# Kernel optimization log

Hardware: AMD Instinct MI355X
Metric: run time of the kernel (lower is better)

Reference implementation:

```python
import jax, jax.numpy as jnp
import numpy as np

B, S, A = 65536, 376, 17
H1, H2, K = 400, 300, 15
MAX_ACTION = 1.0


def setup_inputs() -> dict:
    key = jax.random.key(0)
    ks = jax.random.split(key, 16)

    def lin(kw, fan_in, fan_out):
        lim = 1.0 / np.sqrt(fan_in)
        k1, k2 = jax.random.split(kw)
        W = jax.random.uniform(k1, (fan_in, fan_out), jnp.float32, -lim, lim)
        b = jax.random.uniform(k2, (fan_out,), jnp.float32, -lim, lim)
        return W, b

    W1, b1 = lin(ks[0], S, H1)
    W2, b2 = lin(ks[1], H1, H2)
    Wmu, bmu = lin(ks[2], H2, A)
    Wlv, blv = lin(ks[3], H2, A)
    Wu, bu = lin(ks[4], H2, K * A)
    Ww, bw = lin(ks[5], H2, K * A)
    Wb, bb = lin(ks[6], H2, K)
    x = jax.random.normal(ks[7], (B, S), jnp.float32)
    eps = jax.random.normal(ks[8], (B, A), jnp.float32)
    return dict(x=x, eps=eps, W1=W1, b1=b1, W2=W2, b2=b2, Wmu=Wmu, bmu=bmu,
                Wlv=Wlv, blv=blv, Wu=Wu, bu=bu, Ww=Ww, bw=bw, Wb=Wb, bb=bb)


def _flow_chain(action, u, w, b):
    # u, w: (K, B, A); b: (K, B). Sequential planar flow -> lax.scan over K.
    def step(carry, uwb):
        z, ldj = carry
        u_k, w_k, b_k = uwb
        uw = jnp.sum(w_k * u_k, -1)                       # (B,)
        m_uw = -1.0 + jax.nn.softplus(uw)
        w_norm_sq = jnp.sum(w_k * w_k, -1)
        u_hat = u_k + ((m_uw - uw) / w_norm_sq)[:, None] * w_k  # invertibility reparam
        wzb = jnp.sum(w_k * z, -1) + b_k                  # (B,)
        t = jnp.tanh(wzb)
        z_new = z + u_hat * t[:, None]
        psi_u = jnp.sum(w_k * u_hat, -1) * (1.0 - t * t)  # psi^T u_hat
        ldj_new = ldj + jnp.log(jnp.abs(1.0 + psi_u))
        return (z_new, ldj_new), None

    init = (action, jnp.zeros(action.shape[0], action.dtype))
    (z_fin, ldj), _ = jax.lax.scan(step, init, (u, w, b))
    return z_fin, ldj


def reference(x, eps, W1, b1, W2, b2, Wmu, bmu, Wlv, blv, Wu, bu, Ww, bw, Wb, bb):
    h = jax.nn.relu(x @ W1 + b1)
    h = jax.nn.relu(h @ W2 + b2)
    mu = MAX_ACTION * jnp.tanh(h @ Wmu + bmu)
    log_var = MAX_ACTION * jnp.tanh(h @ Wlv + blv)
    std = jnp.exp(log_var)                 # torch code uses log_var.exp() as the scale
    action = mu + std * eps                # rsample

    u = (h @ Wu + bu).reshape(B, K, A).transpose(1, 0, 2)   # (K, B, A)
    w = (h @ Ww + bw).reshape(B, K, A).transpose(1, 0, 2)   # (K, B, A)
    b = (h @ Wb + bb).T                                      # (K, B)

    final_action, log_det_j = _flow_chain(action, u, w, b)

    # Normal(mu, std).log_prob(action) summed over action dim; (action-mu)/std == eps
    log_2pi = jnp.float32(np.log(2.0 * np.pi))
    log_prob = jnp.sum(-0.5 * eps * eps - log_var - 0.5 * log_2pi, axis=-1)
    log_prob_final = log_prob - log_det_j
    prob_final = jnp.exp(log_prob_final)
    return final_action, prob_final, log_prob_final
```

## Files before the change

kernel.cpp:

```cpp
#include <hip/hip_runtime.h>

typedef unsigned short ushort_t;
typedef unsigned int uint_t;
typedef __bf16 bf16x8 __attribute__((ext_vector_type(8)));
typedef float f32x4 __attribute__((ext_vector_type(4)));

#define B_ROWS 65536

#define KT1 12
#define NT1 30
#define KTC1 15
#define KI2 13
#define NT2 20
#define KTC2 10
#define KI3 10
#define NT3 40
#define LDC3 640

#define SZ1 (NT1 * KT1 * 512)
#define SZ2 (NT2 * KI2 * 512)
#define SZ3 (NT3 * KI3 * 512)

__device__ inline float bf2f(ushort_t u) {
    union { uint_t i; float f; } x; x.i = ((uint_t)u) << 16; return x.f;
}
__device__ inline ushort_t f2bf(float f) {
    uint_t u = __float_as_uint(f);
    return (ushort_t)((u + 0x7FFFu + ((u >> 16) & 1u)) >> 16);
}
__device__ inline uint_t pack2(float a, float b) {
    return (uint_t)f2bf(a) | ((uint_t)f2bf(b) << 16);
}
__device__ inline float fast_tanh(float x) {
    float e = __expf(2.f * x);
    return 1.f - 2.f / (e + 1.f);
}
__device__ inline void gl2lds16(const ushort_t* g, ushort_t* l) {
    __builtin_amdgcn_global_load_lds(
        (const __attribute__((address_space(1))) uint_t*)g,
        (__attribute__((address_space(3))) uint_t*)l, 16, 0, 0);
}

__global__ void pack_kernel(const float* __restrict__ W1, const float* __restrict__ W2,
                            const float* __restrict__ Wmu, const float* __restrict__ Wlv,
                            const float* __restrict__ Wu, const float* __restrict__ Ww,
                            const float* __restrict__ Wb,
                            const float* __restrict__ b1, const float* __restrict__ b2,
                            const float* __restrict__ bmu, const float* __restrict__ blv,
                            const float* __restrict__ bu, const float* __restrict__ bw,
                            const float* __restrict__ bb,
                            ushort_t* __restrict__ W1t, ushort_t* __restrict__ W2t,
                            ushort_t* __restrict__ Wht,
                            float* __restrict__ b1p, float* __restrict__ b2p,
                            float* __restrict__ bHp)
{
    int i = blockIdx.x * 256 + threadIdx.x;
    if (i < SZ1) {
        int t = i >> 9, pos = i & 511;
        int l = pos >> 3, j = pos & 7;
        int n = (t / KT1) * 16 + (l & 15);
        int k = (t % KT1) * 32 + (l >> 4) * 8 + j;
        W1t[i] = (n < 400 && k < 376) ? f2bf(W1[k * 400 + n]) : (ushort_t)0;
    } else if (i < SZ1 + SZ2) {
        int i2 = i - SZ1;
        int t = i2 >> 9, pos = i2 & 511;
        int l = pos >> 3, j = pos & 7;
        int n = (t / KI2) * 16 + (l & 15);
        int k = (t % KI2) * 32 + (l >> 4) * 8 + j;
        W2t[i2] = (n < 300 && k < 400) ? f2bf(W2[k * 300 + n]) : (ushort_t)0;
    } else if (i < SZ1 + SZ2 + SZ3) {
        int i3 = i - SZ1 - SZ2;
        int t = i3 >> 9, pos = i3 & 511;
        int l = pos >> 3, j = pos & 7;
        int n = (t / KI3) * 16 + (l & 15);
        int k = (t % KI3) * 32 + (l >> 4) * 8 + j;
        float v = 0.f;
        if (k < 300) {
            if      (n < 17)  v = Wmu[k * 17 + n];
            else if (n < 34)  v = Wlv[k * 17 + (n - 17)];
            else if (n < 289) v = Wu[k * 255 + (n - 34)];
            else if (n < 544) v = Ww[k * 255 + (n - 289)];
            else if (n < 559) v = Wb[k * 15 + (n - 544)];
        }
        Wht[i3] = f2bf(v);
    } else {
        int j = i - SZ1 - SZ2 - SZ3;
        if (j < 480) {
            b1p[j] = (j < 400) ? b1[j] : 0.f;
        } else if (j < 800) {
            int n = j - 480;
            b2p[n] = (n < 300) ? b2[n] : 0.f;
        } else if (j < 1440) {
            int n = j - 800;
            float v = 0.f;
            if      (n < 17)  v = bmu[n];
            else if (n < 34)  v = blv[n - 17];
            else if (n < 289) v = bu[n - 34];
            else if (n < 544) v = bw[n - 289];
            else if (n < 559) v = bb[n - 544];
            bHp[n] = v;
        }
    }
}

__global__ __launch_bounds__(256)
void cvt_kernel(const float* __restrict__ x, ushort_t* __restrict__ xt, int nUnits)
{
    int U = blockIdx.x * 256 + threadIdx.x;
    if (U >= nUnits) return;
    int t = U >> 6, l = U & 63;
    int rowblk = t / KT1, kblk = t - rowblk * KT1;
    long row = (long)rowblk * 16 + (l & 15);
    int k0 = kblk * 32 + (l >> 4) * 8;
    uint4 o = {0u, 0u, 0u, 0u};
    if (k0 + 8 <= 376) {
        const float4* p = reinterpret_cast<const float4*>(x + row * 376 + k0);
        float4 v0 = p[0], v1 = p[1];
        o.x = pack2(v0.x, v0.y); o.y = pack2(v0.z, v0.w);
        o.z = pack2(v1.x, v1.y); o.w = pack2(v1.z, v1.w);
    }
    reinterpret_cast<uint4*>(xt)[U] = o;
}

template<bool RELU, bool OUT_TILED>
__global__ __launch_bounds__(256)
void gemm_tile(const ushort_t* __restrict__ A, const ushort_t* __restrict__ Bt,
               const float* __restrict__ bias, ushort_t* __restrict__ C,
               int kTA, int kIters, int kTC)
{
    __shared__ ushort_t As[8 * 512];
    __shared__ ushort_t Bs[10 * 512];
    const int tid = threadIdx.x;
    const int lane = tid & 63, wv = tid >> 6;
    const int q = lane >> 4, l16 = lane & 15;
    const int nb0 = blockIdx.x * 10;
    const int rowblk0 = blockIdx.y * 8;

    f32x4 acc[2][10];
    #pragma unroll
    for (int r = 0; r < 2; ++r)
        #pragma unroll
        for (int c = 0; c < 10; ++c)
            acc[r][c] = (f32x4){0.f, 0.f, 0.f, 0.f};

    for (int kt = 0; kt < kIters; ++kt) {
        #pragma unroll
        for (int i = 0; i < 2; ++i) {
            int t = wv * 2 + i;
            gl2lds16(A + (((size_t)(rowblk0 + t) * kTA + kt) << 9) + lane * 8,
                     &As[t << 9]);
        }
        #pragma unroll
        for (int t2 = 0; t2 < 3; ++t2) {
            int t = wv + t2 * 4;
            if (t < 10)
                gl2lds16(Bt + (((size_t)(nb0 + t) * kIters + kt) << 9) + lane * 8,
                         &Bs[t << 9]);
        }
        __syncthreads();

        bf16x8 a0 = __builtin_bit_cast(bf16x8,
            *reinterpret_cast<const uint4*>(&As[((wv * 2 + 0) << 9) + lane * 8]));
        bf16x8 a1 = __builtin_bit_cast(bf16x8,
            *reinterpret_cast<const uint4*>(&As[((wv * 2 + 1) << 9) + lane * 8]));
        #pragma unroll
        for (int c = 0; c < 10; ++c) {
            bf16x8 b = __builtin_bit_cast(bf16x8,
                *reinterpret_cast<const uint4*>(&Bs[(c << 9) + lane * 8]));
            acc[0][c] = __builtin_amdgcn_mfma_f32_16x16x32_bf16(a0, b, acc[0][c], 0, 0, 0);
            acc[1][c] = __builtin_amdgcn_mfma_f32_16x16x32_bf16(a1, b, acc[1][c], 0, 0, 0);
        }
        __syncthreads();
    }

    #pragma unroll
    for (int r = 0; r < 2; ++r) {
        int rowblk = rowblk0 + wv * 2 + r;
        #pragma unroll
        for (int c = 0; c < 10; ++c) {
            int n = (nb0 + c) * 16 + l16;
            float bv = bias[n];
            #pragma unroll
            for (int reg = 0; reg < 4; ++reg) {
                float v = acc[r][c][reg] + bv;
                if (RELU) v = fmaxf(v, 0.f);
                int mrow = q * 4 + reg;
                if (OUT_TILED) {
                    size_t off = (((size_t)rowblk * kTC + (n >> 5)) << 9)
                               + (size_t)(((n >> 3) & 3) * 16 + mrow) * 8 + (n & 7);
                    C[off] = f2bf(v);
                } else {
                    long m = (long)rowblk * 16 + mrow;
                    C[m * (long)kTC + n] = f2bf(v);
                }
            }
        }
    }
}

#define FR 128

__global__ __launch_bounds__(FR)
void flow_kernel(const ushort_t* __restrict__ heads, const float* __restrict__ eps,
                 float* __restrict__ out, int rowBase, int B)
{
    __shared__ float lu[17 * (FR + 1)];
    __shared__ float lw[17 * (FR + 1)];
    __shared__ float le[17 * (FR + 1)];
    __shared__ float lb[FR];
    const int tid = threadIdx.x;
    const long row0 = (long)blockIdx.x * FR;
    const ushort_t* hbase = heads + row0 * LDC3;

    for (int idx = tid; idx < FR * 17; idx += FR) {
        int r = idx / 17, i = idx - r * 17;
        lu[i * (FR + 1) + r] = bf2f(hbase[(long)r * LDC3 + i]);
        lw[i * (FR + 1) + r] = bf2f(hbase[(long)r * LDC3 + 17 + i]);
        le[i * (FR + 1) + r] = eps[row0 * 17 + idx];
    }
    __syncthreads();

    float z[17];
    float lp = 0.f;
    #pragma unroll
    for (int i = 0; i < 17; ++i) {
        float mu = fast_tanh(lu[i * (FR + 1) + tid]);
        float lv = fast_tanh(lw[i * (FR + 1) + tid]);
        float ep = le[i * (FR + 1) + tid];
        z[i] = mu + __expf(lv) * ep;
        lp += -0.5f * ep * ep - lv - 0.918938533f;
    }

    float ldj = 0.f;
    for (int k = 0; k < 15; ++k) {
        __syncthreads();
        for (int idx = tid; idx < FR * 17; idx += FR) {
            int r = idx / 17, i = idx - r * 17;
            long rb = (long)r * LDC3;
            lu[i * (FR + 1) + r] = bf2f(hbase[rb + 34 + k * 17 + i]);
            lw[i * (FR + 1) + r] = bf2f(hbase[rb + 289 + k * 17 + i]);
        }
        lb[tid] = bf2f(hbase[(long)tid * LDC3 + 544 + k]);
        __syncthreads();

        float u[17], w[17];
        float uw = 0.f, w2 = 0.f, wz = 0.f;
        #pragma unroll
        for (int i = 0; i < 17; ++i) {
            u[i] = lu[i * (FR + 1) + tid];
            w[i] = lw[i * (FR + 1) + tid];
            uw += w[i] * u[i];
            w2 += w[i] * w[i];
            wz += w[i] * z[i];
        }
        float sp = (uw > 15.f) ? uw : __logf(1.f + __expf(uw));
        float m = sp - 1.f;
        float coef = (m - uw) / fmaxf(w2, 1e-20f);
        float t = fast_tanh(wz + lb[tid]);
        #pragma unroll
        for (int i = 0; i < 17; ++i)
            z[i] += (u[i] + coef * w[i]) * t;
        float psi = m * (1.f - t * t);
        ldj += __logf(fmaxf(fabsf(1.f + psi), 1e-30f));
    }

    const long g = rowBase + row0 + tid;
    #pragma unroll
    for (int i = 0; i < 17; ++i) out[g * 17 + i] = z[i];
    float lpf = lp - ldj;
    out[(long)B * 17 + g] = __expf(lpf);
    out[(long)B * 18 + g] = lpf;
}

extern "C" void kernel_launch(void* const* d_in, const int* in_sizes, int n_in,
                              void* d_out, int out_size, void* d_ws, size_t ws_size,
                              hipStream_t stream)
{
    const float* x   = (const float*)d_in[0];
    const float* eps = (const float*)d_in[1];
    float* out = (float*)d_out;

    const size_t wUS = (size_t)SZ1 + SZ2 + SZ3;
    const size_t fixedBytes = wUS * 2 + (480 + 320 + 640) * 4;
    int Mc = 2048;
    {
        const int cand[6] = {65536, 32768, 16384, 8192, 4096, 2048};
        for (int i = 0; i < 6; ++i) {
            size_t req = (size_t)cand[i] * 2048 + fixedBytes;
            if (req <= ws_size) { Mc = cand[i]; break; }
        }
    }

    ushort_t* region1 = (ushort_t*)d_ws;
    ushort_t* region2 = region1 + (size_t)Mc * 640;
    ushort_t* W1t = region2 + (size_t)Mc * 384;
    ushort_t* W2t = W1t + SZ1;
    ushort_t* Wht = W2t + SZ2;
    float* b1p = (float*)(Wht + SZ3);
    float* b2p = b1p + 480;
    float* bHp = b2p + 320;

    const int packN = SZ1 + SZ2 + SZ3 + 1440;
    pack_kernel<<<(packN + 255) / 256, 256, 0, stream>>>(
        (const float*)d_in[2],  (const float*)d_in[4],
        (const float*)d_in[6],  (const float*)d_in[8],
        (const float*)d_in[10], (const float*)d_in[12], (const float*)d_in[14],
        (const float*)d_in[3],  (const float*)d_in[5],
        (const float*)d_in[7],  (const float*)d_in[9],
        (const float*)d_in[11], (const float*)d_in[13], (const float*)d_in[15],
        W1t, W2t, Wht, b1p, b2p, bHp);

    const int nChunks = B_ROWS / Mc;
    const int nUnits = Mc * 48;
    for (int c = 0; c < nChunks; ++c) {
        const float* xc = x + (size_t)c * Mc * 376;
        cvt_kernel<<<(nUnits + 255) / 256, 256, 0, stream>>>(xc, region2, nUnits);
        gemm_tile<true, true><<<dim3(3, Mc / 128), 256, 0, stream>>>(
            region2, W1t, b1p, region1, KT1, KT1, KTC1);
        gemm_tile<true, true><<<dim3(2, Mc / 128), 256, 0, stream>>>(
            region1, W2t, b2p, region2, KTC1, KI2, KTC2);
        gemm_tile<false, false><<<dim3(4, Mc / 128), 256, 0, stream>>>(
            region2, Wht, bHp, region1, KTC2, KI3, LDC3);
        flow_kernel<<<Mc / FR, FR, 0, stream>>>(region1, eps + (size_t)c * Mc * 17,
                                                out, c * Mc, B_ROWS);
    }
}
```

Before: 375.8 us.

## Write head GEMM output in tiled layout and read it per-thread in flow kernel

The head GEMM now stores its output in the same tiled bf16 layout used by the earlier layers instead of a row-major 640-wide matrix. The flow kernel reads that layout directly: each thread loads 16-byte groups of 8 bf16 values for its own row. This replaces the shared-memory staging and the per-step __syncthreads. Each thread loads slightly more data than it needs (three groups per 17-element slice), and the fully unrolled K loop with 24-float buffers raises register pressure.

```diff
diff --git a/kernel.cpp b/kernel.cpp
--- a/kernel.cpp
+++ b/kernel.cpp
@@ -15,7 +15,7 @@
 #define KTC2 10
 #define KI3 10
 #define NT3 40
-#define LDC3 640
+#define LDH3 20
 
 #define SZ1 (NT1 * KT1 * 512)
 #define SZ2 (NT2 * KI2 * 512)
@@ -198,78 +198,85 @@
     }
 }
 
-#define FR 128
-
-__global__ __launch_bounds__(FR)
+__device__ inline void ld_group8(const ushort_t* hb, int g, float* dst) {
+    uint4 v = *reinterpret_cast<const uint4*>(hb + ((g >> 2) << 9) + ((g & 3) << 7));
+    uint_t q[4] = {v.x, v.y, v.z, v.w};
+    #pragma unroll
+    for (int m = 0; m < 4; ++m) {
+        dst[2 * m]     = __uint_as_float(q[m] << 16);
+        dst[2 * m + 1] = __uint_as_float(q[m] & 0xFFFF0000u);
+    }
+}
+
+__global__ __launch_bounds__(64)
 void flow_kernel(const ushort_t* __restrict__ heads, const float* __restrict__ eps,
-                 float* __restrict__ out, int rowBase, int B)
-{
-    __shared__ float lu[17 * (FR + 1)];
-    __shared__ float lw[17 * (FR + 1)];
-    __shared__ float le[17 * (FR + 1)];
-    __shared__ float lb[FR];
+                 float* __restrict__ out, int rowBase, int Btot)
+{
     const int tid = threadIdx.x;
-    const long row0 = (long)blockIdx.x * FR;
-    const ushort_t* hbase = heads + row0 * LDC3;
-
-    for (int idx = tid; idx < FR * 17; idx += FR) {
-        int r = idx / 17, i = idx - r * 17;
-        lu[i * (FR + 1) + r] = bf2f(hbase[(long)r * LDC3 + i]);
-        lw[i * (FR + 1) + r] = bf2f(hbase[(long)r * LDC3 + 17 + i]);
-        le[i * (FR + 1) + r] = eps[row0 * 17 + idx];
-    }
-    __syncthreads();
+    const long row = (long)blockIdx.x * 64 + tid;
+    const ushort_t* hb = heads + (((size_t)(row >> 4) * LDH3) << 9)
+                               + (size_t)((row & 15) << 3);
 
     float z[17];
     float lp = 0.f;
-    #pragma unroll
-    for (int i = 0; i < 17; ++i) {
-        float mu = fast_tanh(lu[i * (FR + 1) + tid]);
-        float lv = fast_tanh(lw[i * (FR + 1) + tid]);
-        float ep = le[i * (FR + 1) + tid];
-        z[i] = mu + __expf(lv) * ep;
-        lp += -0.5f * ep * ep - lv - 0.918938533f;
-    }
+    {
+        float a[40];
+        #pragma unroll
+        for (int g = 0; g < 5; ++g) ld_group8(hb, g, &a[g * 8]);
+        #pragma unroll
+        for (int i = 0; i < 17; ++i) {
+            float mu = fast_tanh(a[i]);
+            float lv = fast_tanh(a[17 + i]);
+            float ep = eps[row * 17 + i];
+            z[i] = mu + __expf(lv) * ep;
+            lp += -0.5f * ep * ep - lv - 0.918938533f;
+        }
+    }
+
+    float bv[16];
+    ld_group8(hb, 68, &bv[0]);
+    ld_group8(hb, 69, &bv[8]);
 
     float ldj = 0.f;
+    #pragma unroll
     for (int k = 0; k < 15; ++k) {
-        __syncthreads();
-        for (int idx = tid; idx < FR * 17; idx += FR) {
-            int r = idx / 17, i = idx - r * 17;
-            long rb = (long)r * LDC3;
-            lu[i * (FR + 1) + r] = bf2f(hbase[rb + 34 + k * 17 + i]);
-            lw[i * (FR + 1) + r] = bf2f(hbase[rb + 289 + k * 17 + i]);
-        }
-        lb[tid] = bf2f(hbase[(long)tid * LDC3 + 544 + k]);
-        __syncthreads();
-
-        float u[17], w[17];
+        const int su = 34 + 17 * k;
+        const int sw = 289 + 17 * k;
+        const int gu = su >> 3, ou = su & 7;
+        const int gw = sw >> 3, ow = sw & 7;
+        float au[24], aw[24];
+        ld_group8(hb, gu + 0, &au[0]);
+        ld_group8(hb, gu + 1, &au[8]);
+        ld_group8(hb, gu + 2, &au[16]);
+        ld_group8(hb, gw + 0, &aw[0]);
+        ld_group8(hb, gw + 1, &aw[8]);
+        ld_group8(hb, gw + 2, &aw[16]);
+
         float uw = 0.f, w2 = 0.f, wz = 0.f;
         #pragma unroll
         for (int i = 0; i < 17; ++i) {
-            u[i] = lu[i * (FR + 1) + tid];
-            w[i] = lw[i * (FR + 1) + tid];
-            uw += w[i] * u[i];
-            w2 += w[i] * w[i];
-            wz += w[i] * z[i];
+            float wi = aw[ow + i], ui = au[ou + i];
+            uw += wi * ui;
+            w2 += wi * wi;
+            wz += wi * z[i];
         }
         float sp = (uw > 15.f) ? uw : __logf(1.f + __expf(uw));
         float m = sp - 1.f;
         float coef = (m - uw) / fmaxf(w2, 1e-20f);
-        float t = fast_tanh(wz + lb[tid]);
+        float t = fast_tanh(wz + bv[k]);
         #pragma unroll
         for (int i = 0; i < 17; ++i)
-            z[i] += (u[i] + coef * w[i]) * t;
+            z[i] += (au[ou + i] + coef * aw[ow + i]) * t;
         float psi = m * (1.f - t * t);
         ldj += __logf(fmaxf(fabsf(1.f + psi), 1e-30f));
     }
 
-    const long g = rowBase + row0 + tid;
+    const long g = rowBase + row;
     #pragma unroll
     for (int i = 0; i < 17; ++i) out[g * 17 + i] = z[i];
     float lpf = lp - ldj;
-    out[(long)B * 17 + g] = __expf(lpf);
-    out[(long)B * 18 + g] = lpf;
+    out[(long)Btot * 17 + g] = __expf(lpf);
+    out[(long)Btot * 18 + g] = lpf;
 }
 
 extern "C" void kernel_launch(void* const* d_in, const int* in_sizes, int n_in,
@@ -319,9 +326,9 @@
             region2, W1t, b1p, region1, KT1, KT1, KTC1);
         gemm_tile<true, true><<<dim3(2, Mc / 128), 256, 0, stream>>>(
             region1, W2t, b2p, region2, KTC1, KI2, KTC2);
-        gemm_tile<false, false><<<dim3(4, Mc / 128), 256, 0, stream>>>(
-            region2, Wht, bHp, region1, KTC2, KI3, LDC3);
-        flow_kernel<<<Mc / FR, FR, 0, stream>>>(region1, eps + (size_t)c * Mc * 17,
+        gemm_tile<false, true><<<dim3(4, Mc / 128), 256, 0, stream>>>(
+            region2, Wht, bHp, region1, KTC2, KI3, LDH3);
+        flow_kernel<<<Mc / 64, 64, 0, stream>>>(region1, eps + (size_t)c * Mc * 17,
                                                 out, c * Mc, B_ROWS);
     }
 }
```

After: 381.2 us. Within noise of the previous version (+1.4%).
